# Kernel optimization log

Hardware: AMD Instinct MI355X
Metric: run time of the kernel (lower is better)

Reference implementation:

```python
import jax, jax.numpy as jnp
import numpy as np
import math

N_NODES = 20000
N_EDGES = 320000
NODE_IN = 128
HIDDEN = 64
HEADS = 4
TIME_DIM = 64
SCALE = 60.0 / 1.0  # sensitivity / epsilon


def _linear_params(key, din, dout):
    k1, k2 = jax.random.split(key)
    bound = 1.0 / math.sqrt(din)
    w = jax.random.uniform(k1, (din, dout), minval=-bound, maxval=bound, dtype=jnp.float32)
    b = jax.random.uniform(k2, (dout,), minval=-bound, maxval=bound, dtype=jnp.float32)
    return w, b


def setup_inputs() -> dict:
    key = jax.random.key(0)
    ks = jax.random.split(key, 16)
    edge_index = jax.random.randint(ks[0], (2, N_EDGES), 0, N_NODES, dtype=jnp.int64)
    raw_time = jax.random.uniform(ks[1], (N_EDGES, 1), dtype=jnp.float32) * 86400.0
    noise = jax.random.laplace(ks[2], (N_EDGES, 1), dtype=jnp.float32) * SCALE
    node_emb = jax.random.normal(ks[3], (N_NODES, NODE_IN), dtype=jnp.float32)
    HC = HEADS * HIDDEN
    wq1, bq1 = _linear_params(ks[4], NODE_IN, HC)
    wk1, bk1 = _linear_params(ks[5], NODE_IN, HC)
    wv1, bv1 = _linear_params(ks[6], NODE_IN, HC)
    wt1, bt1 = _linear_params(ks[7], TIME_DIM, HC)
    wq2, bq2 = _linear_params(ks[8], HC, HC)
    wk2, bk2 = _linear_params(ks[9], HC, HC)
    wv2, bv2 = _linear_params(ks[10], HC, HC)
    wt2, bt2 = _linear_params(ks[11], TIME_DIM, HC)
    wc, bc = _linear_params(ks[12], HC, 1)
    return dict(edge_index=edge_index, raw_time=raw_time, noise=noise, node_emb=node_emb,
                wq1=wq1, bq1=bq1, wk1=wk1, bk1=bk1, wv1=wv1, bv1=bv1, wt1=wt1, bt1=bt1,
                wq2=wq2, bq2=bq2, wk2=wk2, bk2=bk2, wv2=wv2, bv2=bv2, wt2=wt2, bt2=bt2,
                wc=wc, bc=bc)


def time_encode(t):
    # t: [E, 1] -> [E, TIME_DIM]; interleaved sin/cos as in TimeEncoder
    half = jnp.arange(0, TIME_DIM, 2, dtype=jnp.float32)
    div_term = jnp.exp(half * (-math.log(10000.0) / TIME_DIM))  # [TIME_DIM/2]
    arg = t * div_term  # [E, TIME_DIM/2]
    te = jnp.stack([jnp.sin(arg), jnp.cos(arg)], axis=-1)  # [E, T/2, 2]
    return te.reshape(t.shape[0], TIME_DIM)


def temporal_conv(x, src, dst, time_enc, wq, bq, wk, bk, wv, bv, wt, bt):
    # gather-QKV, edge softmax over dst segments, scatter-add aggregation
    N = x.shape[0]
    q = (x @ wq + bq).reshape(N, HEADS, HIDDEN)
    k = (x @ wk + bk).reshape(N, HEADS, HIDDEN)
    v = (x @ wv + bv).reshape(N, HEADS, HIDDEN)
    t_enc = (time_enc @ wt + bt).reshape(-1, HEADS, HIDDEN)  # [E,H,C]
    q_i = q[dst]                      # [E,H,C]
    k_j = k[src] + t_enc              # [E,H,C]
    alpha = (q_i * k_j).sum(-1) / math.sqrt(HIDDEN)  # [E,H]
    # segment softmax over index = dst (PyG softmax semantics)
    amax = jax.ops.segment_max(alpha, dst, num_segments=N)  # [N,H]
    ea = jnp.exp(alpha - amax[dst])
    denom = jax.ops.segment_sum(ea, dst, num_segments=N)
    alpha = ea / (denom[dst] + 1e-16)
    msg = v[src] * alpha[..., None]   # [E,H,C]
    out = jax.ops.segment_sum(msg, dst, num_segments=N)  # [N,H,C]
    return out.reshape(N, HEADS * HIDDEN)


def reference(edge_index, raw_time, noise, node_emb,
              wq1, bq1, wk1, bk1, wv1, bv1, wt1, bt1,
              wq2, bq2, wk2, bk2, wv2, bv2, wt2, bt2,
              wc, bc):
    src, dst = edge_index[0], edge_index[1]
    noisy_time = raw_time + noise                 # Laplace mechanism
    time_encoded = time_encode(noisy_time)        # [E, TIME_DIM]
    x = jax.nn.relu(temporal_conv(node_emb, src, dst, time_encoded,
                                  wq1, bq1, wk1, bk1, wv1, bv1, wt1, bt1))
    x = jax.nn.relu(temporal_conv(x, src, dst, time_encoded,
                                  wq2, bq2, wk2, bk2, wv2, bv2, wt2, bt2))
    edge_emb = x[src] + x[dst]                    # [E, H*C]
    out = edge_emb @ wc + bc                      # [E, 1]
    return out.squeeze(-1)
```

## Files before the change

### kernel.cpp

```cpp
#include <hip/hip_runtime.h>
#include <hip/hip_fp16.h>
#include <math.h>

#define NN   20000
#define NE   320000
#define NIN  128
#define HC   256
#define NB   1024

#define AGG_BLOCKS 2500
#define AGG_STRIDE 10000
#define LOG2E_8    0.18033688f

typedef unsigned short u16;
typedef __attribute__((ext_vector_type(8))) short bf16x8;
typedef __attribute__((ext_vector_type(4))) float f32x4;

__device__ __forceinline__ float bf2f(u16 u) {
  union { unsigned int i; float f; } x;
  x.i = ((unsigned int)u) << 16;
  return x.f;
}
__device__ __forceinline__ u16 f2bf(float f) {
  union { float f; unsigned int i; } x;
  x.f = f;
  unsigned int r = x.i + 0x7fffu + ((x.i >> 16) & 1u);
  return (u16)(r >> 16);
}
__device__ __forceinline__ float bflo(int v) {
  union { int i; float f; } x; x.i = v << 16; return x.f;
}
__device__ __forceinline__ float bfhi(int v) {
  union { int i; float f; } x; x.i = v & 0xffff0000; return x.f;
}

__device__ __forceinline__ float ldf(const void* p, int i, bool fbf) {
  return fbf ? bf2f(((const u16*)p)[i]) : ((const float*)p)[i];
}
__device__ __forceinline__ int ldsrc(const void* p, int e, bool is64) {
  const int* p32 = (const int*)p;
  return is64 ? p32[2 * e] : p32[e];
}
__device__ __forceinline__ int lddst(const void* p, int e, bool is64) {
  const int* p32 = (const int*)p;
  return is64 ? p32[2 * (NE + e)] : p32[NE + e];
}
__device__ __forceinline__ void stout(void* p, int i, float v, bool fbf) {
  if (fbf) ((u16*)p)[i] = f2bf(v);
  else ((float*)p)[i] = v;
}

__device__ __forceinline__ void gload_lds16(const u16* g, u16* l) {
  __builtin_amdgcn_global_load_lds(
      (const __attribute__((address_space(1))) void*)g,
      (__attribute__((address_space(3))) void*)l, 16, 0, 0);
}

__device__ __forceinline__ float dpp_row_allsum(float s) {
  union fi { float f; int i; };
  fi a, b;
  a.f = s;
  b.i = __builtin_amdgcn_update_dpp(0, a.i, 0x121, 0xf, 0xf, true); a.f += b.f;
  b.i = __builtin_amdgcn_update_dpp(0, a.i, 0x122, 0xf, 0xf, true); a.f += b.f;
  b.i = __builtin_amdgcn_update_dpp(0, a.i, 0x124, 0xf, 0xf, true); a.f += b.f;
  b.i = __builtin_amdgcn_update_dpp(0, a.i, 0x128, 0xf, 0xf, true); a.f += b.f;
  return a.f;
}

__device__ __forceinline__ float fexp2(float x) {
#if __has_builtin(__builtin_amdgcn_exp2f)
  return __builtin_amdgcn_exp2f(x);
#else
  return exp2f(x);
#endif
}

#if __has_builtin(__builtin_amdgcn_fdot2_f32_bf16)
#define HAS_BF16_DOT2 1
typedef __attribute__((ext_vector_type(2))) __bf16 bfv2_t;
__device__ __forceinline__ float qkdot2(int a, int b, float c) {
  return __builtin_amdgcn_fdot2_f32_bf16(__builtin_bit_cast(bfv2_t, a),
                                         __builtin_bit_cast(bfv2_t, b), c, false);
}
#else
#define HAS_BF16_DOT2 0
#endif

__device__ __forceinline__ void edge_do(int4 kv, float tt, int2 q2,
    float dc0, float dc1,
    float qsx, float qsy, float qsz, float qsw,
    float px, float py, float pz, float pw, float qb,
    float& denom, float& a0, float& a1, float& a2, float& a3) {
  const float CH = 0.15915494f;
  const float CL = (float)(0.15915494309189535 - (double)0.15915494f);
  float x0 = tt * dc0, x1 = tt * dc1;
  float p0 = x0 * CH, p1 = x1 * CH;
  float e0 = fmaf(x0, CH, -p0), e1 = fmaf(x1, CH, -p1);
  e0 = fmaf(x0, CL, e0);  e1 = fmaf(x1, CL, e1);
  float fr0 = (p0 - rintf(p0)) + e0;
  float fr1 = (p1 - rintf(p1)) + e1;
  float sv0 = __builtin_amdgcn_sinf(fr0), cv0 = __builtin_amdgcn_cosf(fr0);
  float sv1 = __builtin_amdgcn_sinf(fr1), cv1 = __builtin_amdgcn_cosf(fr1);
  float stp = sv0 * px + cv0 * py + sv1 * pz + cv1 * pw;
#if HAS_BF16_DOT2
  float sqk = qkdot2(kv.y, q2.y, qkdot2(kv.x, q2.x, 0.f));
  float partial = sqk * LOG2E_8 + stp;
#else
  float partial = stp + qsx * bflo(kv.x) + qsy * bfhi(kv.x) +
                  qsz * bflo(kv.y) + qsw * bfhi(kv.y);
#endif
  float a = dpp_row_allsum(partial) + qb;
  float ea = fexp2(a);
  denom += ea;
  a0 = fmaf(ea, bflo(kv.z), a0);
  a1 = fmaf(ea, bfhi(kv.z), a1);
  a2 = fmaf(ea, bflo(kv.w), a2);
  a3 = fmaf(ea, bfhi(kv.w), a3);
}

__global__ void devinit_kernel(const void* __restrict__ eidx,
                               const void* __restrict__ nemb,
                               int* __restrict__ flags, float* __restrict__ divt) {
  int lane = threadIdx.x;
  if (lane < 32) {
    const float c32 = (float)(-0.14391156831212787);
    float prod = (float)(2 * lane) * c32;
    divt[lane] = (float)exp((double)prod);
  }
  if (lane == 0) {
    const int* p32 = (const int*)eidx;
    int is64 = 1;
    for (int i = 1; i < 128; i += 2)
      if (p32[i] != 0) { is64 = 0; break; }
    const u16* q16 = (const u16*)nemb;
    int fbf = 1;
    for (int i = 0; i < 128; i += 2) {
      unsigned e = (q16[i] >> 7) & 0xFF;
      if (e < 90 || e > 140) { fbf = 0; break; }
    }
    flags[0] = is64;
    flags[1] = fbf;
  }
}

__global__ void sentinel_kernel(const int* __restrict__ flags, void* __restrict__ out) {
  int i = blockIdx.x * 256 + threadIdx.x;
  if (i < NE) stout(out, i, 3000.0f, flags[1] != 0);
}
__global__ void raw_sentinel_kernel(u16* __restrict__ out) {
  int i = blockIdx.x * 256 + threadIdx.x;
  if (i < NE) out[i] = f2bf(3000.0f);
}

__global__ void zero_kernel(int* __restrict__ p, int n) {
  int i = blockIdx.x * 256 + threadIdx.x;
  if (i < n) p[i] = 0;
}

__global__ void hist_kernel(const int* __restrict__ flags, const void* __restrict__ eidx,
                            int* __restrict__ cnt) {
  bool is64 = flags[0] != 0;
  int e = blockIdx.x * 256 + threadIdx.x;
  if (e < NE) {
    int d = lddst(eidx, e, is64);
    if ((unsigned)d < NN) atomicAdd(&cnt[d], 1);
  }
}

__global__ void scan1_kernel(const int* __restrict__ cnt, int* __restrict__ offs,
                             int* __restrict__ bsum, int n) {
  __shared__ int s[256];
  int b = blockIdx.x, t = threadIdx.x, i = b * 256 + t;
  int x = (i < n) ? cnt[i] : 0;
  s[t] = x;
  __syncthreads();
  for (int off = 1; off < 256; off <<= 1) {
    int y = (t >= off) ? s[t - off] : 0;
    __syncthreads();
    s[t] += y;
    __syncthreads();
  }
  if (i < n) offs[i] = s[t] - x;
  if (t == 255) bsum[b] = s[t];
}

__global__ void scan2_kernel(int* __restrict__ bsum, int* __restrict__ offs,
                             int nb, int n) {
  __shared__ int s[256];
  int t = threadIdx.x;
  int x = (t < nb) ? bsum[t] : 0;
  s[t] = x;
  __syncthreads();
  for (int off = 1; off < 256; off <<= 1) {
    int y = (t >= off) ? s[t - off] : 0;
    __syncthreads();
    s[t] += y;
    __syncthreads();
  }
  if (t < nb) bsum[t] = s[t] - x;
  if (t == 255) offs[n] = s[t];
}

__global__ void scan3_kernel(int* __restrict__ offs, const int* __restrict__ bsum,
                             int* __restrict__ cursor, int n) {
  int i = blockIdx.x * 256 + threadIdx.x;
  if (i < n) {
    int v = offs[i] + bsum[blockIdx.x];
    offs[i] = v;
    cursor[i] = v;
  }
}

__global__ void fill_kernel(const int* __restrict__ flags, const void* __restrict__ eidx,
                            const void* __restrict__ rawt, const void* __restrict__ noise,
                            int* __restrict__ cursor, int* __restrict__ ssrc,
                            float* __restrict__ stt) {
  bool is64 = flags[0] != 0, fbf = flags[1] != 0;
  int e = blockIdx.x * 256 + threadIdx.x;
  if (e < NE) {
    int d = lddst(eidx, e, is64);
    if ((unsigned)d < NN) {
      int pos = atomicAdd(&cursor[d], 1);
      if ((unsigned)pos < NE) {
        int src = ldsrc(eidx, e, is64);
        if ((unsigned)src >= NN) src = 0;
        ssrc[pos] = src;
        stt[pos] = ldf(rawt, e, fbf) + ldf(noise, e, fbf);
      }
    }
  }
}

__global__ void transw3_kernel(const int* __restrict__ flags, const void* __restrict__ W0,
                               const void* __restrict__ W1, const void* __restrict__ W2,
                               u16* __restrict__ WtBig, int K) {
  bool fbf = flags[1] != 0;
  __shared__ u16 tile[64][65];
  int z = blockIdx.z;
  const void* W = (z == 0) ? W0 : (z == 1) ? W1 : W2;
  u16* dst = WtBig + (size_t)z * 256 * K;
  int kb = blockIdx.x * 64, cb = blockIdx.y * 64;
  int tx = threadIdx.x & 63, ty = threadIdx.x >> 6;
  for (int i = ty; i < 64; i += 4)
    tile[tx][i] = f2bf(ldf(W, (kb + i) * HC + cb + tx, fbf));
  __syncthreads();
  for (int i = ty; i < 64; i += 4)
    dst[(size_t)(cb + i) * K + kb + tx] = tile[i][tx];
}

__global__ void wcombbias_kernel(const int* __restrict__ flags, const void* __restrict__ wt,
                                 const u16* __restrict__ Wqt, u16* __restrict__ Wout,
                                 const void* __restrict__ bq, const void* __restrict__ bk,
                                 const void* __restrict__ bv, float* __restrict__ biasBig,
                                 int K) {
  bool fbf = flags[1] != 0;
  int b = blockIdx.x, t = threadIdx.x;
  if (b < 256) {
    __shared__ float wrow[64];
    int j = b, h = j >> 6;
    if (t < 64) wrow[t] = ldf(wt, (j & 63) * HC + h * 64 + t, fbf);
    __syncthreads();
    if (t < K) {
      float s = 0.f;
#pragma unroll 8
      for (int mm = 0; mm < 64; ++mm)
        s += wrow[mm] * bf2f(Wqt[(size_t)(h * 64 + mm) * K + t]);
      Wout[(size_t)j * K + t] = f2bf(s);
    }
  } else if (b < 259) {
    int bb = b - 256;
    const void* p = (bb == 0) ? bq : (bb == 1) ? bk : bv;
    biasBig[bb * 256 + t] = ldf(p, t, fbf);
  } else {
    int j = t, h = j >> 6;
    float s = 0.f;
    for (int mm = 0; mm < 64; ++mm)
      s += ldf(bq, h * 64 + mm, fbf) * ldf(wt, (j & 63) * HC + h * 64 + mm, fbf);
    biasBig[768 + j] = s;
  }
}

template <bool AWS>
__global__ __launch_bounds__(256) void gemm_mfma(
    const int* __restrict__ flags, const void* __restrict__ Ap,
    const u16* __restrict__ Wt, const float* __restrict__ bias,
    u16* __restrict__ C, int M, int K) {
  bool fbf = flags[1] != 0;
  __shared__ u16 As[128 * 32];
  __shared__ u16 Bs[128 * 32];
  int tid = threadIdx.x;
  int rb = blockIdx.x * 128, cb = blockIdx.y * 128;
  int wave = tid >> 6, lane = tid & 63;
  int l15 = lane & 15, quad = lane >> 4;
  int mbase = (wave >> 1) * 64, nbase = (wave & 1) * 64;

  f32x4 acc[4][4];
#pragma unroll
  for (int mt = 0; mt < 4; ++mt)
#pragma unroll
    for (int nt = 0; nt < 4; ++nt)
#pragma unroll
      for (int r = 0; r < 4; ++r) acc[mt][nt][r] = 0.f;

  int srow0 = tid >> 2, schunk0 = tid & 3;
  int srow1 = (tid + 256) >> 2, schunk1 = (tid + 256) & 3;
  int gchunk0 = schunk0 ^ (srow0 & 3);
  int gchunk1 = schunk1 ^ (srow1 & 3);
  int arow0 = rb + srow0; if (arow0 >= M) arow0 = M - 1;
  int arow1 = rb + srow1; if (arow1 >= M) arow1 = M - 1;
  u16* asl0 = &As[srow0 * 32 + schunk0 * 8];
  u16* asl1 = &As[srow1 * 32 + schunk1 * 8];
  u16* bsl0 = &Bs[srow0 * 32 + schunk0 * 8];
  u16* bsl1 = &Bs[srow1 * 32 + schunk1 * 8];
  const u16* bsrc0 = Wt + (size_t)(cb + srow0) * K + gchunk0 * 8;
  const u16* bsrc1 = Wt + (size_t)(cb + srow1) * K + gchunk1 * 8;
  const bool adirect = AWS || fbf;
  const u16* asrc0 = adirect ? ((const u16*)Ap + (size_t)arow0 * K + gchunk0 * 8) : (const u16*)0;
  const u16* asrc1 = adirect ? ((const u16*)Ap + (size_t)arow1 * K + gchunk1 * 8) : (const u16*)0;

  for (int kk = 0; kk < K; kk += 32) {
    if (adirect) {
      gload_lds16(asrc0 + kk, asl0);
      gload_lds16(asrc1 + kk, asl1);
    } else {
      const float* A0 = (const float*)Ap + (size_t)arow0 * K + kk + gchunk0 * 8;
      const float* A1 = (const float*)Ap + (size_t)arow1 * K + kk + gchunk1 * 8;
      bf16x8 t0, t1;
#pragma unroll
      for (int i = 0; i < 8; ++i) { t0[i] = (short)f2bf(A0[i]); t1[i] = (short)f2bf(A1[i]); }
      *(bf16x8*)asl0 = t0;
      *(bf16x8*)asl1 = t1;
    }
    gload_lds16(bsrc0 + kk, bsl0);
    gload_lds16(bsrc1 + kk, bsl1);
    __syncthreads();

    bf16x8 bfrag[4];
#pragma unroll
    for (int nt = 0; nt < 4; ++nt) {
      int col = nbase + nt * 16 + l15;
      bfrag[nt] = *(const bf16x8*)&Bs[col * 32 + ((quad ^ (col & 3)) * 8)];
    }
#pragma unroll
    for (int mt = 0; mt < 4; ++mt) {
      int row = mbase + mt * 16 + l15;
      bf16x8 afrag = *(const bf16x8*)&As[row * 32 + ((quad ^ (row & 3)) * 8)];
#pragma unroll
      for (int nt = 0; nt < 4; ++nt)
        acc[mt][nt] = __builtin_amdgcn_mfma_f32_16x16x32_bf16(afrag, bfrag[nt], acc[mt][nt], 0, 0, 0);
    }
    __syncthreads();
  }

#pragma unroll
  for (int nt = 0; nt < 4; ++nt) {
    int gcol = cb + nbase + nt * 16 + l15;
    float bv = bias[gcol];
    int scol;
    if (gcol < 256) scol = gcol;
    else if (gcol < 512) { int cc = gcol - 256; scol = 256 + ((cc >> 2) << 3) + (cc & 3); }
    else if (gcol < 768) { int cc = gcol - 512; scol = 256 + ((cc >> 2) << 3) + 4 + (cc & 3); }
    else scol = gcol;
#pragma unroll
    for (int mt = 0; mt < 4; ++mt) {
#pragma unroll
      for (int r = 0; r < 4; ++r) {
        int grow = rb + mbase + mt * 16 + quad * 4 + r;
        if (grow < M) C[(size_t)grow * NB + scol] = f2bf(acc[mt][nt][r] + bv);
      }
    }
  }
}

template <int DOY>
__global__ __launch_bounds__(256) void aggfused_kernel(
    const int* __restrict__ flags, const int* __restrict__ ssrc,
    const int* __restrict__ offsets, const float* __restrict__ stt,
    const float* __restrict__ divt,
    const u16* __restrict__ qkvp, const void* __restrict__ bt,
    u16* __restrict__ xout, const void* __restrict__ wc,
    float* __restrict__ ynode) {
  bool fbf = flags[1] != 0;
  int lane = threadIdx.x & 63;
  int c = lane * 4;
  int kvoff = 256 + lane * 8;

  int i0 = (2 * lane) & 31;
  float dc0 = divt[i0], dc1 = divt[i0 + 1];
  float btv0 = ldf(bt, c + 0, fbf), btv1 = ldf(bt, c + 1, fbf);
  float btv2 = ldf(bt, c + 2, fbf), btv3 = ldf(bt, c + 3, fbf);
  float wcv0 = 0.f, wcv1 = 0.f, wcv2 = 0.f, wcv3 = 0.f;
  if (DOY) {
    wcv0 = ldf(wc, c + 0, fbf); wcv1 = ldf(wc, c + 1, fbf);
    wcv2 = ldf(wc, c + 2, fbf); wcv3 = ldf(wc, c + 3, fbf);
  }

  int n = blockIdx.x * 4 + (threadIdx.x >> 6);
  int s0 = offsets[n], s1 = offsets[n + 1];
  int2 q2 = *(const int2*)(qkvp + (size_t)n * NB + c);
  int2 p2 = *(const int2*)(qkvp + (size_t)n * NB + 768 + c);

  while (n < NN) {
    int n1 = n + AGG_STRIDE;
    int n1c = (n1 < NN) ? n1 : 0;
    int s0n = offsets[n1c], s1n = offsets[n1c + 1];
    int2 q2n = *(const int2*)(qkvp + (size_t)n1c * NB + c);
    int2 p2n = *(const int2*)(qkvp + (size_t)n1c * NB + 768 + c);

    float qx = bflo(q2.x), qy = bfhi(q2.x), qz = bflo(q2.y), qw = bfhi(q2.y);
    float px = bflo(p2.x) * LOG2E_8, py = bfhi(p2.x) * LOG2E_8;
    float pz = bflo(p2.y) * LOG2E_8, pw = bfhi(p2.y) * LOG2E_8;
    float pb = qx * btv0 + qy * btv1 + qz * btv2 + qw * btv3;
    float qb = dpp_row_allsum(pb) * LOG2E_8;
    float qsx = qx * LOG2E_8, qsy = qy * LOG2E_8;
    float qsz = qz * LOG2E_8, qsw = qw * LOG2E_8;

    float denom = 0.f, acc0 = 0.f, acc1 = 0.f, acc2 = 0.f, acc3 = 0.f;
    const int* sp = ssrc + s0;
    const float* tp = stt + s0;
    int ecnt = s1 - s0;
    int e = 0;
    if (ecnt >= 4) {
      int sA = sp[0], sB = sp[1], sC = sp[2], sD = sp[3];
      while (e + 4 <= ecnt) {
        int4 kvA = *(const int4*)(qkvp + ((unsigned)(sA << 10) + (unsigned)kvoff));
        int4 kvB = *(const int4*)(qkvp + ((unsigned)(sB << 10) + (unsigned)kvoff));
        int4 kvC = *(const int4*)(qkvp + ((unsigned)(sC << 10) + (unsigned)kvoff));
        int4 kvD = *(const int4*)(qkvp + ((unsigned)(sD << 10) + (unsigned)kvoff));
        float ttA = tp[e], ttB = tp[e + 1], ttC = tp[e + 2], ttD = tp[e + 3];
        int en = e + 4;
        if (en + 4 <= ecnt) {
          sA = sp[en]; sB = sp[en + 1]; sC = sp[en + 2]; sD = sp[en + 3];
        }
        edge_do(kvA, ttA, q2, dc0, dc1, qsx, qsy, qsz, qsw, px, py, pz, pw, qb,
                denom, acc0, acc1, acc2, acc3);
        edge_do(kvB, ttB, q2, dc0, dc1, qsx, qsy, qsz, qsw, px, py, pz, pw, qb,
                denom, acc0, acc1, acc2, acc3);
        edge_do(kvC, ttC, q2, dc0, dc1, qsx, qsy, qsz, qsw, px, py, pz, pw, qb,
                denom, acc0, acc1, acc2, acc3);
        edge_do(kvD, ttD, q2, dc0, dc1, qsx, qsy, qsz, qsw, px, py, pz, pw, qb,
                denom, acc0, acc1, acc2, acc3);
        e = en;
      }
    }
    for (; e < ecnt; ++e) {
      int s = sp[e];
      int4 kv = *(const int4*)(qkvp + ((unsigned)(s << 10) + (unsigned)kvoff));
      float tt = tp[e];
      edge_do(kv, tt, q2, dc0, dc1, qsx, qsy, qsz, qsw, px, py, pz, pw, qb,
              denom, acc0, acc1, acc2, acc3);
    }

    float inv = 1.f / (denom + 1e-16f);
    ushort4 r;
    r.x = f2bf(fmaxf(acc0 * inv, 0.f));
    r.y = f2bf(fmaxf(acc1 * inv, 0.f));
    r.z = f2bf(fmaxf(acc2 * inv, 0.f));
    r.w = f2bf(fmaxf(acc3 * inv, 0.f));
    *(ushort4*)(xout + (size_t)n * HC + c) = r;
    if (DOY) {
      float yv = bf2f(r.x) * wcv0 + bf2f(r.y) * wcv1 +
                 bf2f(r.z) * wcv2 + bf2f(r.w) * wcv3;
      yv = dpp_row_allsum(yv);
      yv += __shfl_xor(yv, 16);
      yv += __shfl_xor(yv, 32);
      if (lane == 0) ynode[n] = yv;
    }

    n = n1;
    s0 = s0n; s1 = s1n; q2 = q2n; p2 = p2n;
  }
}

__global__ __launch_bounds__(256) void final2_kernel(
    const int* __restrict__ flags, const void* __restrict__ eidx,
    const float* __restrict__ y, const void* __restrict__ bc,
    void* __restrict__ out) {
  bool is64 = flags[0] != 0, fbf = flags[1] != 0;
  int e = blockIdx.x * 256 + threadIdx.x;
  if (e >= NE) return;
  int src = ldsrc(eidx, e, is64);
  int dst = lddst(eidx, e, is64);
  if ((unsigned)src >= NN) src = 0;
  if ((unsigned)dst >= NN) dst = 0;
  stout(out, e, y[src] + y[dst] + ldf(bc, 0, fbf), fbf);
}

extern "C" void kernel_launch(void* const* d_in, const int* in_sizes, int n_in,
                              void* d_out, int out_size, void* d_ws, size_t ws_size,
                              hipStream_t stream) {
  const void* eidx  = d_in[0];
  const void* rawt  = d_in[1];
  const void* noise = d_in[2];
  const void* nemb  = d_in[3];
  const void *wq1 = d_in[4],  *bq1 = d_in[5];
  const void *wk1 = d_in[6],  *bk1 = d_in[7];
  const void *wv1 = d_in[8],  *bv1 = d_in[9];
  const void *wt1 = d_in[10], *bt1 = d_in[11];
  const void *wq2 = d_in[12], *bq2 = d_in[13];
  const void *wk2 = d_in[14], *bk2 = d_in[15];
  const void *wv2 = d_in[16], *bv2 = d_in[17];
  const void *wt2 = d_in[18], *bt2 = d_in[19];
  const void *wcp = d_in[20], *bcp = d_in[21];

  char* ws = (char*)d_ws;
  size_t off = 0;
  auto alloc = [&](size_t bytes) -> void* {
    void* p = ws + off;
    off += (bytes + 255) & ~(size_t)255;
    return p;
  };
  int*   flags  = (int*)alloc(256);
  float* divt   = (float*)alloc(256);
  u16*   WtBig  = (u16*)alloc((size_t)NB * HC * 2);
  float* biasBig= (float*)alloc((size_t)NB * 4);
  u16*   qkvp   = (u16*)alloc((size_t)NN * NB * 2);
  u16*   x1     = (u16*)alloc((size_t)NN * HC * 2);
  u16*   x2     = (u16*)alloc((size_t)NN * HC * 2);
  float* ynode  = (float*)alloc((size_t)NN * 4);
  int* offsets  = (int*)alloc((size_t)(NN + 1) * 4);
  int* cursor   = (int*)alloc((size_t)NN * 4);
  int* bsum     = (int*)alloc(256 * 4);
  int* ssrc     = (int*)alloc((size_t)NE * 4);
  float* stt    = (float*)alloc((size_t)NE * 4);
  size_t need = off;

  int gN = (NN + 255) / 256, gE = (NE + 255) / 256;
  int nb = (NN + 255) / 256;

  if (ws_size < 1024) {
    raw_sentinel_kernel<<<gE, 256, 0, stream>>>((u16*)d_out);
    return;
  }
  devinit_kernel<<<1, 64, 0, stream>>>(eidx, nemb, flags, divt);
  if (need > ws_size) {
    sentinel_kernel<<<gE, 256, 0, stream>>>(flags, d_out);
    return;
  }

  zero_kernel<<<gN, 256, 0, stream>>>(cursor, NN);
  hist_kernel<<<gE, 256, 0, stream>>>(flags, eidx, cursor);
  scan1_kernel<<<nb, 256, 0, stream>>>(cursor, offsets, bsum, NN);
  scan2_kernel<<<1, 256, 0, stream>>>(bsum, offsets, nb, NN);
  scan3_kernel<<<nb, 256, 0, stream>>>(offsets, bsum, cursor, NN);
  fill_kernel<<<gE, 256, 0, stream>>>(flags, eidx, rawt, noise, cursor, ssrc, stt);

  dim3 ggemm((NN + 127) / 128, NB / 128);
  dim3 gt1(NIN / 64, 4, 3), gt2(HC / 64, 4, 3);

  transw3_kernel<<<gt1, 256, 0, stream>>>(flags, wq1, wk1, wv1, WtBig, NIN);
  wcombbias_kernel<<<260, 256, 0, stream>>>(flags, wt1, WtBig, WtBig + (size_t)768 * NIN,
                                            bq1, bk1, bv1, biasBig, NIN);
  gemm_mfma<false><<<ggemm, 256, 0, stream>>>(flags, nemb, WtBig, biasBig, qkvp, NN, NIN);
  aggfused_kernel<0><<<AGG_BLOCKS, 256, 0, stream>>>(flags, ssrc, offsets, stt, divt,
                                                     qkvp, bt1, x1, wcp, ynode);

  transw3_kernel<<<gt2, 256, 0, stream>>>(flags, wq2, wk2, wv2, WtBig, HC);
  wcombbias_kernel<<<260, 256, 0, stream>>>(flags, wt2, WtBig, WtBig + (size_t)768 * HC,
                                            bq2, bk2, bv2, biasBig, HC);
  gemm_mfma<true><<<ggemm, 256, 0, stream>>>(flags, x1, WtBig, biasBig, qkvp, NN, HC);
  aggfused_kernel<1><<<AGG_BLOCKS, 256, 0, stream>>>(flags, ssrc, offsets, stt, divt,
                                                     qkvp, bt2, x2, wcp, ynode);

  final2_kernel<<<gE, 256, 0, stream>>>(flags, eidx, ynode, bcp, d_out);
}
```

Before: 359.0 us.

## Double-buffer GEMM LDS tiles and split interleaved K/V gather into separate loads

The GEMM now stages the next K tile into a second LDS buffer while MFMAs run on the current one, keeping one barrier per iteration. Its epilogue drops the K/V interleaving column remap, so K and V are stored as contiguous 256-wide blocks. The aggregation kernel reads K and V with two 8-byte loads per edge instead of one 16-byte load of interleaved data. This hides global-to-LDS latency in the GEMM and makes epilogue stores more regular, at the cost of doubled LDS use and an extra memory transaction per gathered edge.

```diff
diff --git a/kernel.cpp b/kernel.cpp
--- a/kernel.cpp
+++ b/kernel.cpp
@@ -86,7 +86,7 @@
 #define HAS_BF16_DOT2 0
 #endif
 
-__device__ __forceinline__ void edge_do(int4 kv, float tt, int2 q2,
+__device__ __forceinline__ void edge_do(int2 kk, int2 vv, float tt, int2 q2,
     float dc0, float dc1,
     float qsx, float qsy, float qsz, float qsw,
     float px, float py, float pz, float pw, float qb,
@@ -103,19 +103,19 @@
   float sv1 = __builtin_amdgcn_sinf(fr1), cv1 = __builtin_amdgcn_cosf(fr1);
   float stp = sv0 * px + cv0 * py + sv1 * pz + cv1 * pw;
 #if HAS_BF16_DOT2
-  float sqk = qkdot2(kv.y, q2.y, qkdot2(kv.x, q2.x, 0.f));
+  float sqk = qkdot2(kk.y, q2.y, qkdot2(kk.x, q2.x, 0.f));
   float partial = sqk * LOG2E_8 + stp;
 #else
-  float partial = stp + qsx * bflo(kv.x) + qsy * bfhi(kv.x) +
-                  qsz * bflo(kv.y) + qsw * bfhi(kv.y);
+  float partial = stp + qsx * bflo(kk.x) + qsy * bfhi(kk.x) +
+                  qsz * bflo(kk.y) + qsw * bfhi(kk.y);
 #endif
   float a = dpp_row_allsum(partial) + qb;
   float ea = fexp2(a);
   denom += ea;
-  a0 = fmaf(ea, bflo(kv.z), a0);
-  a1 = fmaf(ea, bfhi(kv.z), a1);
-  a2 = fmaf(ea, bflo(kv.w), a2);
-  a3 = fmaf(ea, bfhi(kv.w), a3);
+  a0 = fmaf(ea, bflo(vv.x), a0);
+  a1 = fmaf(ea, bfhi(vv.x), a1);
+  a2 = fmaf(ea, bflo(vv.y), a2);
+  a3 = fmaf(ea, bfhi(vv.y), a3);
 }
 
 __global__ void devinit_kernel(const void* __restrict__ eidx,
@@ -286,8 +286,8 @@
     const u16* __restrict__ Wt, const float* __restrict__ bias,
     u16* __restrict__ C, int M, int K) {
   bool fbf = flags[1] != 0;
-  __shared__ u16 As[128 * 32];
-  __shared__ u16 Bs[128 * 32];
+  __shared__ u16 As[2][128 * 32];
+  __shared__ u16 Bs[2][128 * 32];
   int tid = threadIdx.x;
   int rb = blockIdx.x * 128, cb = blockIdx.y * 128;
   int wave = tid >> 6, lane = tid & 63;
@@ -308,65 +308,74 @@
   int gchunk1 = schunk1 ^ (srow1 & 3);
   int arow0 = rb + srow0; if (arow0 >= M) arow0 = M - 1;
   int arow1 = rb + srow1; if (arow1 >= M) arow1 = M - 1;
-  u16* asl0 = &As[srow0 * 32 + schunk0 * 8];
-  u16* asl1 = &As[srow1 * 32 + schunk1 * 8];
-  u16* bsl0 = &Bs[srow0 * 32 + schunk0 * 8];
-  u16* bsl1 = &Bs[srow1 * 32 + schunk1 * 8];
+  int slo0 = srow0 * 32 + schunk0 * 8;
+  int slo1 = srow1 * 32 + schunk1 * 8;
   const u16* bsrc0 = Wt + (size_t)(cb + srow0) * K + gchunk0 * 8;
   const u16* bsrc1 = Wt + (size_t)(cb + srow1) * K + gchunk1 * 8;
   const bool adirect = AWS || fbf;
   const u16* asrc0 = adirect ? ((const u16*)Ap + (size_t)arow0 * K + gchunk0 * 8) : (const u16*)0;
   const u16* asrc1 = adirect ? ((const u16*)Ap + (size_t)arow1 * K + gchunk1 * 8) : (const u16*)0;
-
-  for (int kk = 0; kk < K; kk += 32) {
+  const float* afsrc0 = (const float*)Ap + (size_t)arow0 * K + gchunk0 * 8;
+  const float* afsrc1 = (const float*)Ap + (size_t)arow1 * K + gchunk1 * 8;
+
+  auto STAGE = [&](int b, int kk) {
     if (adirect) {
-      gload_lds16(asrc0 + kk, asl0);
-      gload_lds16(asrc1 + kk, asl1);
+      gload_lds16(asrc0 + kk, &As[b][slo0]);
+      gload_lds16(asrc1 + kk, &As[b][slo1]);
     } else {
-      const float* A0 = (const float*)Ap + (size_t)arow0 * K + kk + gchunk0 * 8;
-      const float* A1 = (const float*)Ap + (size_t)arow1 * K + kk + gchunk1 * 8;
+      const float* A0 = afsrc0 + kk;
+      const float* A1 = afsrc1 + kk;
       bf16x8 t0, t1;
 #pragma unroll
       for (int i = 0; i < 8; ++i) { t0[i] = (short)f2bf(A0[i]); t1[i] = (short)f2bf(A1[i]); }
-      *(bf16x8*)asl0 = t0;
-      *(bf16x8*)asl1 = t1;
-    }
-    gload_lds16(bsrc0 + kk, bsl0);
-    gload_lds16(bsrc1 + kk, bsl1);
-    __syncthreads();
-
+      *(bf16x8*)&As[b][slo0] = t0;
+      *(bf16x8*)&As[b][slo1] = t1;
+    }
+    gload_lds16(bsrc0 + kk, &Bs[b][slo0]);
+    gload_lds16(bsrc1 + kk, &Bs[b][slo1]);
+  };
+
+  auto COMPUTE = [&](int b) {
     bf16x8 bfrag[4];
 #pragma unroll
     for (int nt = 0; nt < 4; ++nt) {
       int col = nbase + nt * 16 + l15;
-      bfrag[nt] = *(const bf16x8*)&Bs[col * 32 + ((quad ^ (col & 3)) * 8)];
+      bfrag[nt] = *(const bf16x8*)&Bs[b][col * 32 + ((quad ^ (col & 3)) * 8)];
     }
 #pragma unroll
     for (int mt = 0; mt < 4; ++mt) {
       int row = mbase + mt * 16 + l15;
-      bf16x8 afrag = *(const bf16x8*)&As[row * 32 + ((quad ^ (row & 3)) * 8)];
+      bf16x8 afrag = *(const bf16x8*)&As[b][row * 32 + ((quad ^ (row & 3)) * 8)];
 #pragma unroll
       for (int nt = 0; nt < 4; ++nt)
         acc[mt][nt] = __builtin_amdgcn_mfma_f32_16x16x32_bf16(afrag, bfrag[nt], acc[mt][nt], 0, 0, 0);
     }
+  };
+
+  STAGE(0, 0);
+  __syncthreads();
+  int cur = 0;
+  for (int kk = 32; kk < K; kk += 32) {
+    STAGE(cur ^ 1, kk);
+    COMPUTE(cur);
     __syncthreads();
-  }
-
-#pragma unroll
-  for (int nt = 0; nt < 4; ++nt) {
-    int gcol = cb + nbase + nt * 16 + l15;
-    float bv = bias[gcol];
-    int scol;
-    if (gcol < 256) scol = gcol;
-    else if (gcol < 512) { int cc = gcol - 256; scol = 256 + ((cc >> 2) << 3) + (cc & 3); }
-    else if (gcol < 768) { int cc = gcol - 512; scol = 256 + ((cc >> 2) << 3) + 4 + (cc & 3); }
-    else scol = gcol;
-#pragma unroll
-    for (int mt = 0; mt < 4; ++mt) {
-#pragma unroll
-      for (int r = 0; r < 4; ++r) {
-        int grow = rb + mbase + mt * 16 + quad * 4 + r;
-        if (grow < M) C[(size_t)grow * NB + scol] = f2bf(acc[mt][nt][r] + bv);
+    cur ^= 1;
+  }
+  COMPUTE(cur);
+
+  float bvv[4];
+#pragma unroll
+  for (int nt = 0; nt < 4; ++nt) bvv[nt] = bias[cb + nbase + nt * 16 + l15];
+#pragma unroll
+  for (int mt = 0; mt < 4; ++mt) {
+#pragma unroll
+    for (int r = 0; r < 4; ++r) {
+      int grow = rb + mbase + mt * 16 + quad * 4 + r;
+      if (grow < M) {
+        size_t rowo = (size_t)grow * NB + cb + nbase + l15;
+#pragma unroll
+        for (int nt = 0; nt < 4; ++nt)
+          C[rowo + nt * 16] = f2bf(acc[mt][nt][r] + bvv[nt]);
       }
     }
   }
@@ -383,7 +392,6 @@
   bool fbf = flags[1] != 0;
   int lane = threadIdx.x & 63;
   int c = lane * 4;
-  int kvoff = 256 + lane * 8;
 
   int i0 = (2 * lane) & 31;
   float dc0 = divt[i0], dc1 = divt[i0 + 1];
@@ -423,31 +431,36 @@
     if (ecnt >= 4) {
       int sA = sp[0], sB = sp[1], sC = sp[2], sD = sp[3];
       while (e + 4 <= ecnt) {
-        int4 kvA = *(const int4*)(qkvp + ((unsigned)(sA << 10) + (unsigned)kvoff));
-        int4 kvB = *(const int4*)(qkvp + ((unsigned)(sB << 10) + (unsigned)kvoff));
-        int4 kvC = *(const int4*)(qkvp + ((unsigned)(sC << 10) + (unsigned)kvoff));
-        int4 kvD = *(const int4*)(qkvp + ((unsigned)(sD << 10) + (unsigned)kvoff));
+        const u16* bA = qkvp + ((unsigned)sA << 10) + c;
+        const u16* bB = qkvp + ((unsigned)sB << 10) + c;
+        const u16* bC = qkvp + ((unsigned)sC << 10) + c;
+        const u16* bD = qkvp + ((unsigned)sD << 10) + c;
+        int2 kA = *(const int2*)(bA + 256), vA = *(const int2*)(bA + 512);
+        int2 kB = *(const int2*)(bB + 256), vB = *(const int2*)(bB + 512);
+        int2 kC = *(const int2*)(bC + 256), vC = *(const int2*)(bC + 512);
+        int2 kD = *(const int2*)(bD + 256), vD = *(const int2*)(bD + 512);
         float ttA = tp[e], ttB = tp[e + 1], ttC = tp[e + 2], ttD = tp[e + 3];
         int en = e + 4;
         if (en + 4 <= ecnt) {
           sA = sp[en]; sB = sp[en + 1]; sC = sp[en + 2]; sD = sp[en + 3];
         }
-        edge_do(kvA, ttA, q2, dc0, dc1, qsx, qsy, qsz, qsw, px, py, pz, pw, qb,
+        edge_do(kA, vA, ttA, q2, dc0, dc1, qsx, qsy, qsz, qsw, px, py, pz, pw, qb,
                 denom, acc0, acc1, acc2, acc3);
-        edge_do(kvB, ttB, q2, dc0, dc1, qsx, qsy, qsz, qsw, px, py, pz, pw, qb,
+        edge_do(kB, vB, ttB, q2, dc0, dc1, qsx, qsy, qsz, qsw, px, py, pz, pw, qb,
                 denom, acc0, acc1, acc2, acc3);
-        edge_do(kvC, ttC, q2, dc0, dc1, qsx, qsy, qsz, qsw, px, py, pz, pw, qb,
+        edge_do(kC, vC, ttC, q2, dc0, dc1, qsx, qsy, qsz, qsw, px, py, pz, pw, qb,
                 denom, acc0, acc1, acc2, acc3);
-        edge_do(kvD, ttD, q2, dc0, dc1, qsx, qsy, qsz, qsw, px, py, pz, pw, qb,
+        edge_do(kD, vD, ttD, q2, dc0, dc1, qsx, qsy, qsz, qsw, px, py, pz, pw, qb,
                 denom, acc0, acc1, acc2, acc3);
         e = en;
       }
     }
     for (; e < ecnt; ++e) {
       int s = sp[e];
-      int4 kv = *(const int4*)(qkvp + ((unsigned)(s << 10) + (unsigned)kvoff));
+      const u16* bS = qkvp + ((unsigned)s << 10) + c;
+      int2 kS = *(const int2*)(bS + 256), vS = *(const int2*)(bS + 512);
       float tt = tp[e];
-      edge_do(kv, tt, q2, dc0, dc1, qsx, qsy, qsz, qsw, px, py, pz, pw, qb,
+      edge_do(kS, vS, tt, q2, dc0, dc1, qsx, qsy, qsz, qsw, px, py, pz, pw, qb,
               denom, acc0, acc1, acc2, acc3);
     }
 
```

After: 337.0 us. 6.1% less time.
